# Performance work log

Measured on AMD Instinct MI355X. Metric: run time of the kernel, lower is better.

## Reference

```python
import jax, jax.numpy as jnp
import numpy as np

N_NODES = 50000
N_EDGES = 300000
D = 256
N_RELS = 500


def setup_inputs() -> dict:
    key = jax.random.key(0)
    ks = jax.random.split(key, 12)
    s = 1.0 / np.sqrt(D)  # keep activations O(1) through the dense transforms
    return {
        "h": jax.random.normal(ks[0], (N_NODES, D), dtype=jnp.float32),
        "prev_h": jax.random.normal(ks[1], (N_NODES, D), dtype=jnp.float32),
        "emb_rel": jax.random.normal(ks[2], (N_RELS, D), dtype=jnp.float32),
        "norm": jax.random.uniform(ks[3], (N_NODES, 1), dtype=jnp.float32),
        "weight_neighbor": jax.random.normal(ks[4], (D, D), dtype=jnp.float32) * s,
        "loop_weight": jax.random.normal(ks[5], (D, D), dtype=jnp.float32) * s,
        "evolve_loop_weight": jax.random.normal(ks[6], (D, D), dtype=jnp.float32) * s,
        "skip_connect_weight": jax.random.normal(ks[7], (D, D), dtype=jnp.float32) * s,
        "skip_connect_bias": jnp.zeros((D,), dtype=jnp.float32),
        "src": jax.random.randint(ks[8], (N_EDGES,), 0, N_NODES),
        "dst": jax.random.randint(ks[9], (N_EDGES,), 0, N_NODES),
        "etype": jax.random.randint(ks[10], (N_EDGES,), 0, N_RELS),
    }


def reference(h, prev_h, emb_rel, norm, weight_neighbor, loop_weight,
              evolve_loop_weight, skip_connect_weight, skip_connect_bias,
              src, dst, etype):
    n_nodes = h.shape[0]
    # msg_func: per-edge gather of src features + relation embedding, dense transform
    msg = (h[src] + emb_rel[etype]) @ weight_neighbor          # [E, D]
    # fn.sum: segment-sum messages into destination nodes
    agg = jax.ops.segment_sum(msg, dst, num_segments=n_nodes)  # [N, D]
    # apply_func: multiply by per-node norm
    agg = agg * norm
    # self-loop: loop_weight where in_degree > 0, evolve_loop_weight otherwise
    in_deg = jax.ops.segment_sum(jnp.ones_like(dst), dst, num_segments=n_nodes)
    has_in = (in_deg > 0)[:, None]
    loop_message = jnp.where(has_in, h @ loop_weight, h @ evolve_loop_weight)
    # skip connection gate
    skip_weight = jax.nn.sigmoid(prev_h @ skip_connect_weight + skip_connect_bias)
    node_repr = skip_weight * (agg + loop_message) + (1.0 - skip_weight) * prev_h
    return jax.nn.relu(node_repr)
```

## Files before the change

kernel.cpp:

```cpp
#include <hip/hip_runtime.h>
#include <hip/hip_bf16.h>
#include <cstdint>
#include <cstddef>

#define N_NODES 50000
#define N_EDGES 300000
#define DIM     256
#define KTOT    768
#define N_RELS  500

#define SCAN_BLK  256
#define SCAN_NBLK ((N_NODES + SCAN_BLK - 1) / SCAN_BLK)

typedef unsigned short u16;
typedef __attribute__((ext_vector_type(8))) short short8v;
typedef __attribute__((ext_vector_type(4))) float float4v;

static __device__ __forceinline__ u16 f2bf(float f) {
    union { float f; unsigned u; } v; v.f = f;
    unsigned u = v.u;
    unsigned r = u + 0x7FFFu + ((u >> 16) & 1u);
    return (u16)(r >> 16);
}
static __device__ __forceinline__ float bf2f(u16 b) {
    union { unsigned u; float f; } v; v.u = ((unsigned)b) << 16; return v.f;
}

__global__ void conv_kernel(const float* __restrict__ h, const float* __restrict__ emb,
                            u16* __restrict__ Xh, u16* __restrict__ embb) {
    int i = blockIdx.x * blockDim.x + threadIdx.x;
    int e0 = i * 8;
    if (e0 >= (N_NODES + N_RELS) * DIM) return;
    const float* src; u16* dst; int off;
    if (e0 < N_NODES * DIM) { src = h;   dst = Xh;   off = e0; }
    else                    { src = emb; dst = embb; off = e0 - N_NODES * DIM; }
    float4 a = *(const float4*)(src + off);
    float4 b = *(const float4*)(src + off + 4);
    u16 o[8] = { f2bf(a.x), f2bf(a.y), f2bf(a.z), f2bf(a.w),
                 f2bf(b.x), f2bf(b.y), f2bf(b.z), f2bf(b.w) };
    *(uint4*)(dst + off) = *(const uint4*)o;
}

__global__ void wt_kernel(const float* __restrict__ Wn, const float* __restrict__ Wl,
                          const float* __restrict__ Wsc, u16* __restrict__ Wt) {
    int k = blockIdx.x;
    int d = threadIdx.x;
    const float* W = (k < 256) ? Wn : ((k < 512) ? Wl : Wsc);
    int kk = k & 255;
    Wt[(size_t)d * KTOT + k] = f2bf(W[kk * DIM + d]);
}

__global__ void hist_kernel(const int* __restrict__ dstv, int* __restrict__ deg) {
    int e = blockIdx.x * 256 + threadIdx.x;
    if (e < N_EDGES) atomicAdd(&deg[dstv[e]], 1);
}

__global__ void scanA_kernel(const int* __restrict__ deg, int* __restrict__ excl_local,
                             int* __restrict__ block_sum) {
    __shared__ int sdata[SCAN_BLK];
    int t = threadIdx.x, i = blockIdx.x * SCAN_BLK + t;
    int v = (i < N_NODES) ? deg[i] : 0;
    sdata[t] = v;
    __syncthreads();
    for (int off = 1; off < SCAN_BLK; off <<= 1) {
        int u = (t >= off) ? sdata[t - off] : 0;
        __syncthreads();
        sdata[t] += u;
        __syncthreads();
    }
    if (i < N_NODES) excl_local[i] = sdata[t] - v;
    if (t == SCAN_BLK - 1) block_sum[blockIdx.x] = sdata[t];
}

__global__ void scanB_kernel(const int* __restrict__ block_sum, int* __restrict__ block_base,
                             int* __restrict__ offsets) {
    __shared__ int sdata[SCAN_NBLK];
    int t = threadIdx.x;
    int v = (t < SCAN_NBLK) ? block_sum[t] : 0;
    if (t < SCAN_NBLK) sdata[t] = v;
    __syncthreads();
    for (int off = 1; off < SCAN_NBLK; off <<= 1) {
        int u = (t >= off && t < SCAN_NBLK) ? sdata[t - off] : 0;
        __syncthreads();
        if (t < SCAN_NBLK) sdata[t] += u;
        __syncthreads();
    }
    if (t < SCAN_NBLK) block_base[t] = sdata[t] - v;
    if (t == SCAN_NBLK - 1) offsets[N_NODES] = sdata[t];
}

__global__ void scanC_kernel(const int* __restrict__ excl_local, const int* __restrict__ block_base,
                             int* __restrict__ offsets, int* __restrict__ cursor) {
    int i = blockIdx.x * SCAN_BLK + threadIdx.x;
    if (i < N_NODES) {
        int e = block_base[blockIdx.x] + excl_local[i];
        offsets[i] = e; cursor[i] = e;
    }
}

__global__ void scatter_kernel(const int* __restrict__ src, const int* __restrict__ dstv,
                               const int* __restrict__ et, int* __restrict__ cursor,
                               unsigned* __restrict__ esee) {
    int e = blockIdx.x * 256 + threadIdx.x;
    if (e >= N_EDGES) return;
    int d = dstv[e];
    int pos = atomicAdd(&cursor[d], 1);
    esee[pos] = (unsigned)src[e] * N_RELS + (unsigned)et[e];
}

__global__ void agg_kernel(const u16* __restrict__ Xh, const u16* __restrict__ embb,
                           const float* __restrict__ norm, const int* __restrict__ offsets,
                           const unsigned* __restrict__ esee,
                           u16* __restrict__ Xa, int* __restrict__ wl_count, int* __restrict__ wl) {
    int wave = (blockIdx.x * 256 + threadIdx.x) >> 6;
    int lane = threadIdx.x & 63;
    if (wave >= N_NODES) return;
    int n = wave;
    int s0 = offsets[n], s1 = offsets[n + 1];
    int c4 = lane * 4;
    float4 acc = make_float4(0.f, 0.f, 0.f, 0.f);
    for (int e = s0; e < s1; e++) {
        unsigned v = esee[e];
        unsigned s = v / N_RELS;
        unsigned t = v - s * N_RELS;
        ushort4 hv = *(const ushort4*)(Xh   + (size_t)s * DIM + c4);
        ushort4 ev = *(const ushort4*)(embb + (size_t)t * DIM + c4);
        acc.x += bf2f(hv.x) + bf2f(ev.x);
        acc.y += bf2f(hv.y) + bf2f(ev.y);
        acc.z += bf2f(hv.z) + bf2f(ev.z);
        acc.w += bf2f(hv.w) + bf2f(ev.w);
    }
    float nr = norm[n];
    u16 o[4] = { f2bf(acc.x * nr), f2bf(acc.y * nr), f2bf(acc.z * nr), f2bf(acc.w * nr) };
    *(ushort4*)(Xa + (size_t)n * DIM + c4) = *(const ushort4*)o;
    if (lane == 0 && s1 == s0) { int idx = atomicAdd(wl_count, 1); wl[idx] = n; }
}

#define LDSP 72
__launch_bounds__(256, 2)
__global__ void gemm_kernel(const u16* __restrict__ Xa, const u16* __restrict__ Xh,
                            const u16* __restrict__ Wt, const float* __restrict__ prev_h,
                            const float* __restrict__ bias, float* __restrict__ out) {
    __shared__ u16 Xs[64 * LDSP];
    __shared__ u16 Ws[256 * LDSP];
    int tid = threadIdx.x;
    int wave = tid >> 6, lane = tid & 63, q = lane >> 4, m16 = lane & 15;
    int wn = wave * 64;
    int m0 = blockIdx.x * 64;

    float4v acc1[4][4], acc2[4][4];
#pragma unroll
    for (int i = 0; i < 4; i++)
#pragma unroll
        for (int j = 0; j < 4; j++) { acc1[i][j] = (float4v)0.f; acc2[i][j] = (float4v)0.f; }

    int xr = tid >> 3, xc = (tid & 7) * 8;
    int wp = tid & 7,  wd = tid >> 3;
    int xrow0 = min(m0 + xr, N_NODES - 1);
    int xrow1 = min(m0 + xr + 32, N_NODES - 1);

    for (int kt = 0; kt < 12; kt++) {
        int koff = (kt & 3) * 64;
        if (kt < 8) {
            const u16* Xsrc = (kt < 4) ? Xa : Xh;
            *(uint4*)(&Xs[xr * LDSP + xc]) =
                *(const uint4*)(Xsrc + (size_t)xrow0 * DIM + koff + xc);
            *(uint4*)(&Xs[(xr + 32) * LDSP + xc]) =
                *(const uint4*)(Xsrc + (size_t)xrow1 * DIM + koff + xc);
        } else {
            const float* p0 = prev_h + (size_t)xrow0 * DIM + koff + xc;
            const float* p1 = prev_h + (size_t)xrow1 * DIM + koff + xc;
            float4 a0 = *(const float4*)p0, b0 = *(const float4*)(p0 + 4);
            float4 a1 = *(const float4*)p1, b1 = *(const float4*)(p1 + 4);
            u16 o0[8] = { f2bf(a0.x), f2bf(a0.y), f2bf(a0.z), f2bf(a0.w),
                          f2bf(b0.x), f2bf(b0.y), f2bf(b0.z), f2bf(b0.w) };
            u16 o1[8] = { f2bf(a1.x), f2bf(a1.y), f2bf(a1.z), f2bf(a1.w),
                          f2bf(b1.x), f2bf(b1.y), f2bf(b1.z), f2bf(b1.w) };
            *(uint4*)(&Xs[xr * LDSP + xc])        = *(const uint4*)o0;
            *(uint4*)(&Xs[(xr + 32) * LDSP + xc]) = *(const uint4*)o1;
        }
#pragma unroll
        for (int it = 0; it < 8; it++) {
            int d = wd + it * 32;
            *(uint4*)(&Ws[d * LDSP + wp * 8]) =
                *(const uint4*)(Wt + (size_t)d * KTOT + kt * 64 + wp * 8);
        }
        __syncthreads();
#pragma unroll
        for (int kk = 0; kk < 2; kk++) {
            short8v af[4], bfr[4];
#pragma unroll
            for (int mi = 0; mi < 4; mi++)
                af[mi] = *(const short8v*)(&Xs[(mi * 16 + m16) * LDSP + kk * 32 + q * 8]);
#pragma unroll
            for (int ni = 0; ni < 4; ni++)
                bfr[ni] = *(const short8v*)(&Ws[(wn + ni * 16 + m16) * LDSP + kk * 32 + q * 8]);
            if (kt < 8) {
#pragma unroll
                for (int mi = 0; mi < 4; mi++)
#pragma unroll
                    for (int ni = 0; ni < 4; ni++)
                        acc1[mi][ni] = __builtin_amdgcn_mfma_f32_16x16x32_bf16(
                            af[mi], bfr[ni], acc1[mi][ni], 0, 0, 0);
            } else {
#pragma unroll
                for (int mi = 0; mi < 4; mi++)
#pragma unroll
                    for (int ni = 0; ni < 4; ni++)
                        acc2[mi][ni] = __builtin_amdgcn_mfma_f32_16x16x32_bf16(
                            af[mi], bfr[ni], acc2[mi][ni], 0, 0, 0);
            }
        }
        __syncthreads();
    }

#pragma unroll
    for (int mi = 0; mi < 4; mi++) {
#pragma unroll
        for (int ni = 0; ni < 4; ni++) {
            int d = wn + ni * 16 + m16;
            float b = bias[d];
#pragma unroll
            for (int r = 0; r < 4; r++) {
                int node = m0 + mi * 16 + q * 4 + r;
                if (node < N_NODES) {
                    float S  = acc2[mi][ni][r] + b;
                    float sw = 1.f / (1.f + __expf(-S));
                    float ph = prev_h[(size_t)node * DIM + d];
                    float v  = sw * acc1[mi][ni][r] + (1.f - sw) * ph;
                    out[(size_t)node * DIM + d] = fmaxf(v, 0.f);
                }
            }
        }
    }
}

__global__ void fixup_kernel(const float* __restrict__ h, const float* __restrict__ prev_h,
                             const float* __restrict__ We, const float* __restrict__ Wsc,
                             const float* __restrict__ bias, const int* __restrict__ wl_count,
                             const int* __restrict__ wl, float* __restrict__ out) {
    __shared__ float ph[DIM], hh[DIM];
    int d = threadIdx.x;
    int cnt = *wl_count;
    for (int i = blockIdx.x; i < cnt; i += gridDim.x) {
        int n = wl[i];
        ph[d] = prev_h[(size_t)n * DIM + d];
        hh[d] = h[(size_t)n * DIM + d];
        __syncthreads();
        float s = 0.f, l = 0.f;
        for (int k = 0; k < DIM; k++) {
            s += ph[k] * Wsc[k * DIM + d];
            l += hh[k] * We[k * DIM + d];
        }
        float sw = 1.f / (1.f + __expf(-(s + bias[d])));
        float v = sw * l + (1.f - sw) * ph[d];
        out[(size_t)n * DIM + d] = fmaxf(v, 0.f);
        __syncthreads();
    }
}

extern "C" void kernel_launch(void* const* d_in, const int* in_sizes, int n_in,
                              void* d_out, int out_size, void* d_ws, size_t ws_size,
                              hipStream_t stream) {
    const float* h      = (const float*)d_in[0];
    const float* prev_h = (const float*)d_in[1];
    const float* emb    = (const float*)d_in[2];
    const float* norm   = (const float*)d_in[3];
    const float* Wn     = (const float*)d_in[4];
    const float* Wl     = (const float*)d_in[5];
    const float* We     = (const float*)d_in[6];
    const float* Wsc    = (const float*)d_in[7];
    const float* bias   = (const float*)d_in[8];
    const int*   src    = (const int*)d_in[9];
    const int*   dstv   = (const int*)d_in[10];
    const int*   et     = (const int*)d_in[11];
    float* out = (float*)d_out;

    char* ws = (char*)d_ws;
    size_t off = 0;
    auto alloc = [&](size_t bytes) -> char* {
        char* p = ws + off; off += (bytes + 255) & ~(size_t)255; return p;
    };
    u16* Xa      = (u16*)alloc((size_t)N_NODES * DIM * 2);
    u16* Xh      = (u16*)alloc((size_t)N_NODES * DIM * 2);
    u16* embb    = (u16*)alloc((size_t)N_RELS * DIM * 2);
    u16* Wt      = (u16*)alloc((size_t)DIM * KTOT * 2);
    int* deg     = (int*)alloc((size_t)N_NODES * 4);
    int* wlcnt   = (int*)alloc(16);
    int* wl      = (int*)alloc((size_t)N_NODES * 4);
    int* offsets = (int*)alloc((size_t)(N_NODES + 1) * 4);
    int* cursor  = (int*)alloc((size_t)N_NODES * 4);
    unsigned* esee = (unsigned*)alloc((size_t)N_EDGES * 4);
    int* excl    = (int*)alloc((size_t)N_NODES * 4);
    int* bsum    = (int*)alloc((size_t)SCAN_NBLK * 4);
    int* bbase   = (int*)alloc((size_t)SCAN_NBLK * 4);

    hipMemsetAsync(deg, 0, (size_t)N_NODES * 4, stream);
    hipMemsetAsync(wlcnt, 0, 4, stream);

    conv_kernel<<<((N_NODES + N_RELS) * DIM / 8 + 255) / 256, 256, 0, stream>>>(h, emb, Xh, embb);
    wt_kernel<<<KTOT, 256, 0, stream>>>(Wn, Wl, Wsc, Wt);
    hist_kernel<<<(N_EDGES + 255) / 256, 256, 0, stream>>>(dstv, deg);
    scanA_kernel<<<SCAN_NBLK, SCAN_BLK, 0, stream>>>(deg, excl, bsum);
    scanB_kernel<<<1, SCAN_BLK, 0, stream>>>(bsum, bbase, offsets);
    scanC_kernel<<<SCAN_NBLK, SCAN_BLK, 0, stream>>>(excl, bbase, offsets, cursor);
    scatter_kernel<<<(N_EDGES + 255) / 256, 256, 0, stream>>>(src, dstv, et, cursor, esee);
    agg_kernel<<<(N_NODES + 3) / 4, 256, 0, stream>>>(Xh, embb, norm, offsets, esee, Xa, wlcnt, wl);
    gemm_kernel<<<(N_NODES + 63) / 64, 256, 0, stream>>>(Xa, Xh, Wt, prev_h, bias, out);
    fixup_kernel<<<256, 256, 0, stream>>>(h, prev_h, We, Wsc, bias, wlcnt, wl, out);
}
```

Measured before the change: 348.5 us.

## Double-buffer GEMM via direct global-to-LDS loads with swizzled layout and concatenated X

Rewrites the fused GEMM main loop to double-buffer LDS tiles, filling them with global_load_lds (direct global-to-LDS copies) and an XOR-swizzled layout in place of padded rows, so the next K-tile loads while MFMAs run on the current one. The prev_h tiles are prefetched into registers and converted after compute. The aggregated and raw node features are stored interleaved in one 512-wide buffer so the A operand comes from a single source. The aggregation loop is also unrolled by two edges to raise memory-level parallelism. LDS use grows because of double buffering, which may limit occupancy, and the swizzle/async-load indexing adds correctness risk.

```diff
diff --git a/kernel.cpp b/kernel.cpp
--- a/kernel.cpp
+++ b/kernel.cpp
@@ -1,5 +1,4 @@
 #include <hip/hip_runtime.h>
-#include <hip/hip_bf16.h>
 #include <cstdint>
 #include <cstddef>
 
@@ -26,19 +25,32 @@
     union { unsigned u; float f; } v; v.u = ((unsigned)b) << 16; return v.f;
 }
 
+static __device__ __forceinline__ void gld16(const void* g, u16* l) {
+    __builtin_amdgcn_global_load_lds(
+        (const __attribute__((address_space(1))) unsigned int*)g,
+        (__attribute__((address_space(3))) unsigned int*)l,
+        16, 0, 0);
+}
+
 __global__ void conv_kernel(const float* __restrict__ h, const float* __restrict__ emb,
-                            u16* __restrict__ Xh, u16* __restrict__ embb) {
+                            u16* __restrict__ Xcat, u16* __restrict__ embb) {
     int i = blockIdx.x * blockDim.x + threadIdx.x;
     int e0 = i * 8;
     if (e0 >= (N_NODES + N_RELS) * DIM) return;
-    const float* src; u16* dst; int off;
-    if (e0 < N_NODES * DIM) { src = h;   dst = Xh;   off = e0; }
-    else                    { src = emb; dst = embb; off = e0 - N_NODES * DIM; }
-    float4 a = *(const float4*)(src + off);
-    float4 b = *(const float4*)(src + off + 4);
+    const float* src; u16* dst;
+    if (e0 < N_NODES * DIM) {
+        int n = e0 >> 8, c = e0 & 255;
+        src = h + e0;
+        dst = Xcat + (size_t)n * 512 + 256 + c;
+    } else {
+        int off = e0 - N_NODES * DIM;
+        src = emb + off; dst = embb + off;
+    }
+    float4 a = *(const float4*)(src);
+    float4 b = *(const float4*)(src + 4);
     u16 o[8] = { f2bf(a.x), f2bf(a.y), f2bf(a.z), f2bf(a.w),
                  f2bf(b.x), f2bf(b.y), f2bf(b.z), f2bf(b.w) };
-    *(uint4*)(dst + off) = *(const uint4*)o;
+    *(uint4*)dst = *(const uint4*)o;
 }
 
 __global__ void wt_kernel(const float* __restrict__ Wn, const float* __restrict__ Wl,
@@ -108,10 +120,10 @@
     esee[pos] = (unsigned)src[e] * N_RELS + (unsigned)et[e];
 }
 
-__global__ void agg_kernel(const u16* __restrict__ Xh, const u16* __restrict__ embb,
+__global__ void agg_kernel(u16* __restrict__ Xcat, const u16* __restrict__ embb,
                            const float* __restrict__ norm, const int* __restrict__ offsets,
                            const unsigned* __restrict__ esee,
-                           u16* __restrict__ Xa, int* __restrict__ wl_count, int* __restrict__ wl) {
+                           int* __restrict__ wl_count, int* __restrict__ wl) {
     int wave = (blockIdx.x * 256 + threadIdx.x) >> 6;
     int lane = threadIdx.x & 63;
     if (wave >= N_NODES) return;
@@ -119,11 +131,25 @@
     int s0 = offsets[n], s1 = offsets[n + 1];
     int c4 = lane * 4;
     float4 acc = make_float4(0.f, 0.f, 0.f, 0.f);
-    for (int e = s0; e < s1; e++) {
+    int e = s0;
+    for (; e + 1 < s1; e += 2) {
+        unsigned v0 = esee[e], v1 = esee[e + 1];
+        unsigned sa = v0 / N_RELS, ta = v0 - sa * N_RELS;
+        unsigned sb = v1 / N_RELS, tb = v1 - sb * N_RELS;
+        ushort4 ha = *(const ushort4*)(Xcat + (size_t)sa * 512 + 256 + c4);
+        ushort4 ea = *(const ushort4*)(embb + (size_t)ta * DIM + c4);
+        ushort4 hb = *(const ushort4*)(Xcat + (size_t)sb * 512 + 256 + c4);
+        ushort4 eb = *(const ushort4*)(embb + (size_t)tb * DIM + c4);
+        acc.x += bf2f(ha.x) + bf2f(ea.x) + bf2f(hb.x) + bf2f(eb.x);
+        acc.y += bf2f(ha.y) + bf2f(ea.y) + bf2f(hb.y) + bf2f(eb.y);
+        acc.z += bf2f(ha.z) + bf2f(ea.z) + bf2f(hb.z) + bf2f(eb.z);
+        acc.w += bf2f(ha.w) + bf2f(ea.w) + bf2f(hb.w) + bf2f(eb.w);
+    }
+    if (e < s1) {
         unsigned v = esee[e];
         unsigned s = v / N_RELS;
         unsigned t = v - s * N_RELS;
-        ushort4 hv = *(const ushort4*)(Xh   + (size_t)s * DIM + c4);
+        ushort4 hv = *(const ushort4*)(Xcat + (size_t)s * 512 + 256 + c4);
         ushort4 ev = *(const ushort4*)(embb + (size_t)t * DIM + c4);
         acc.x += bf2f(hv.x) + bf2f(ev.x);
         acc.y += bf2f(hv.y) + bf2f(ev.y);
@@ -132,21 +158,32 @@
     }
     float nr = norm[n];
     u16 o[4] = { f2bf(acc.x * nr), f2bf(acc.y * nr), f2bf(acc.z * nr), f2bf(acc.w * nr) };
-    *(ushort4*)(Xa + (size_t)n * DIM + c4) = *(const ushort4*)o;
+    *(ushort4*)(Xcat + (size_t)n * 512 + c4) = *(const ushort4*)o;
     if (lane == 0 && s1 == s0) { int idx = atomicAdd(wl_count, 1); wl[idx] = n; }
 }
 
-#define LDSP 72
 __launch_bounds__(256, 2)
-__global__ void gemm_kernel(const u16* __restrict__ Xa, const u16* __restrict__ Xh,
-                            const u16* __restrict__ Wt, const float* __restrict__ prev_h,
-                            const float* __restrict__ bias, float* __restrict__ out) {
-    __shared__ u16 Xs[64 * LDSP];
-    __shared__ u16 Ws[256 * LDSP];
-    int tid = threadIdx.x;
+__global__ void gemm_kernel(const u16* __restrict__ Xcat, const u16* __restrict__ Wt,
+                            const float* __restrict__ prev_h, const float* __restrict__ bias,
+                            float* __restrict__ out) {
+    __shared__ __align__(16) u16 lds[40960];
+    int tid  = threadIdx.x;
     int wave = tid >> 6, lane = tid & 63, q = lane >> 4, m16 = lane & 15;
     int wn = wave * 64;
     int m0 = blockIdx.x * 64;
+    int lr = lane >> 3, lc8 = lane & 7;
+    int scol = (lc8 ^ lr) << 3;
+
+    int ar0 = wave * 16 + lr, ar1 = ar0 + 8;
+    int ga0 = (m0 + ar0 < N_NODES) ? (m0 + ar0) : (N_NODES - 1);
+    int ga1 = (m0 + ar1 < N_NODES) ? (m0 + ar1) : (N_NODES - 1);
+    const u16*   sA0 = Xcat   + (size_t)ga0 * 512 + scol;
+    const u16*   sA1 = Xcat   + (size_t)ga1 * 512 + scol;
+    const float* pP0 = prev_h + (size_t)ga0 * 256 + scol;
+    const float* pP1 = prev_h + (size_t)ga1 * 256 + scol;
+    const u16*   sB  = Wt + (size_t)(wave * 64 + lr) * KTOT + scol;
+    int ldsA_w = wave * 16 * 64;
+    int ldsB_w = 8192 + wave * 64 * 64;
 
     float4v acc1[4][4], acc2[4][4];
 #pragma unroll
@@ -154,47 +191,49 @@
 #pragma unroll
         for (int j = 0; j < 4; j++) { acc1[i][j] = (float4v)0.f; acc2[i][j] = (float4v)0.f; }
 
-    int xr = tid >> 3, xc = (tid & 7) * 8;
-    int wp = tid & 7,  wd = tid >> 3;
-    int xrow0 = min(m0 + xr, N_NODES - 1);
-    int xrow1 = min(m0 + xr + 32, N_NODES - 1);
-
+#pragma unroll
+    for (int j = 0; j < 8; j++)
+        gld16(sB + (size_t)j * 8 * KTOT, &lds[ldsB_w + j * 512]);
+    gld16(sA0, &lds[ldsA_w]);
+    gld16(sA1, &lds[ldsA_w + 512]);
+    __syncthreads();
+
+    int sw = (m16 & 7) << 3;
+
+#pragma unroll
     for (int kt = 0; kt < 12; kt++) {
-        int koff = (kt & 3) * 64;
-        if (kt < 8) {
-            const u16* Xsrc = (kt < 4) ? Xa : Xh;
-            *(uint4*)(&Xs[xr * LDSP + xc]) =
-                *(const uint4*)(Xsrc + (size_t)xrow0 * DIM + koff + xc);
-            *(uint4*)(&Xs[(xr + 32) * LDSP + xc]) =
-                *(const uint4*)(Xsrc + (size_t)xrow1 * DIM + koff + xc);
-        } else {
-            const float* p0 = prev_h + (size_t)xrow0 * DIM + koff + xc;
-            const float* p1 = prev_h + (size_t)xrow1 * DIM + koff + xc;
-            float4 a0 = *(const float4*)p0, b0 = *(const float4*)(p0 + 4);
-            float4 a1 = *(const float4*)p1, b1 = *(const float4*)(p1 + 4);
-            u16 o0[8] = { f2bf(a0.x), f2bf(a0.y), f2bf(a0.z), f2bf(a0.w),
-                          f2bf(b0.x), f2bf(b0.y), f2bf(b0.z), f2bf(b0.w) };
-            u16 o1[8] = { f2bf(a1.x), f2bf(a1.y), f2bf(a1.z), f2bf(a1.w),
-                          f2bf(b1.x), f2bf(b1.y), f2bf(b1.z), f2bf(b1.w) };
-            *(uint4*)(&Xs[xr * LDSP + xc])        = *(const uint4*)o0;
-            *(uint4*)(&Xs[(xr + 32) * LDSP + xc]) = *(const uint4*)o1;
-        }
-#pragma unroll
-        for (int it = 0; it < 8; it++) {
-            int d = wd + it * 32;
-            *(uint4*)(&Ws[d * LDSP + wp * 8]) =
-                *(const uint4*)(Wt + (size_t)d * KTOT + kt * 64 + wp * 8);
-        }
-        __syncthreads();
+        int buf = kt & 1, nbuf = buf ^ 1;
+        float pf0[8], pf1[8];
+        if (kt < 11) {
+            int kn = kt + 1;
+#pragma unroll
+            for (int j = 0; j < 8; j++)
+                gld16(sB + (size_t)j * 8 * KTOT + kn * 64,
+                      &lds[ldsB_w + nbuf * 16384 + j * 512]);
+            if (kn < 8) {
+                gld16(sA0 + kn * 64, &lds[ldsA_w + nbuf * 4096]);
+                gld16(sA1 + kn * 64, &lds[ldsA_w + nbuf * 4096 + 512]);
+            } else {
+                const float* p0 = pP0 + (kn - 8) * 64;
+                const float* p1 = pP1 + (kn - 8) * 64;
+                float4 x0 = *(const float4*)p0, y0 = *(const float4*)(p0 + 4);
+                float4 x1 = *(const float4*)p1, y1 = *(const float4*)(p1 + 4);
+                pf0[0] = x0.x; pf0[1] = x0.y; pf0[2] = x0.z; pf0[3] = x0.w;
+                pf0[4] = y0.x; pf0[5] = y0.y; pf0[6] = y0.z; pf0[7] = y0.w;
+                pf1[0] = x1.x; pf1[1] = x1.y; pf1[2] = x1.z; pf1[3] = x1.w;
+                pf1[4] = y1.x; pf1[5] = y1.y; pf1[6] = y1.z; pf1[7] = y1.w;
+            }
+        }
 #pragma unroll
         for (int kk = 0; kk < 2; kk++) {
+            int ck = (kk * 32 + q * 8) ^ sw;
             short8v af[4], bfr[4];
 #pragma unroll
             for (int mi = 0; mi < 4; mi++)
-                af[mi] = *(const short8v*)(&Xs[(mi * 16 + m16) * LDSP + kk * 32 + q * 8]);
+                af[mi] = *(const short8v*)(&lds[buf * 4096 + (mi * 16 + m16) * 64 + ck]);
 #pragma unroll
             for (int ni = 0; ni < 4; ni++)
-                bfr[ni] = *(const short8v*)(&Ws[(wn + ni * 16 + m16) * LDSP + kk * 32 + q * 8]);
+                bfr[ni] = *(const short8v*)(&lds[8192 + buf * 16384 + (wn + ni * 16 + m16) * 64 + ck]);
             if (kt < 8) {
 #pragma unroll
                 for (int mi = 0; mi < 4; mi++)
@@ -211,6 +250,14 @@
                             af[mi], bfr[ni], acc2[mi][ni], 0, 0, 0);
             }
         }
+        if (kt < 11 && kt + 1 >= 8) {
+            u16 o0[8] = { f2bf(pf0[0]), f2bf(pf0[1]), f2bf(pf0[2]), f2bf(pf0[3]),
+                          f2bf(pf0[4]), f2bf(pf0[5]), f2bf(pf0[6]), f2bf(pf0[7]) };
+            u16 o1[8] = { f2bf(pf1[0]), f2bf(pf1[1]), f2bf(pf1[2]), f2bf(pf1[3]),
+                          f2bf(pf1[4]), f2bf(pf1[5]), f2bf(pf1[6]), f2bf(pf1[7]) };
+            *(uint4*)(&lds[nbuf * 4096 + ar0 * 64 + lc8 * 8]) = *(const uint4*)o0;
+            *(uint4*)(&lds[nbuf * 4096 + ar1 * 64 + lc8 * 8]) = *(const uint4*)o1;
+        }
         __syncthreads();
     }
 
@@ -225,9 +272,9 @@
                 int node = m0 + mi * 16 + q * 4 + r;
                 if (node < N_NODES) {
                     float S  = acc2[mi][ni][r] + b;
-                    float sw = 1.f / (1.f + __expf(-S));
+                    float sg = 1.f / (1.f + __expf(-S));
                     float ph = prev_h[(size_t)node * DIM + d];
-                    float v  = sw * acc1[mi][ni][r] + (1.f - sw) * ph;
+                    float v  = sg * acc1[mi][ni][r] + (1.f - sg) * ph;
                     out[(size_t)node * DIM + d] = fmaxf(v, 0.f);
                 }
             }
@@ -252,8 +299,8 @@
             s += ph[k] * Wsc[k * DIM + d];
             l += hh[k] * We[k * DIM + d];
         }
-        float sw = 1.f / (1.f + __expf(-(s + bias[d])));
-        float v = sw * l + (1.f - sw) * ph[d];
+        float sg = 1.f / (1.f + __expf(-(s + bias[d])));
+        float v = sg * l + (1.f - sg) * ph[d];
         out[(size_t)n * DIM + d] = fmaxf(v, 0.f);
         __syncthreads();
     }
@@ -281,8 +328,7 @@
     auto alloc = [&](size_t bytes) -> char* {
         char* p = ws + off; off += (bytes + 255) & ~(size_t)255; return p;
     };
-    u16* Xa      = (u16*)alloc((size_t)N_NODES * DIM * 2);
-    u16* Xh      = (u16*)alloc((size_t)N_NODES * DIM * 2);
+    u16* Xcat    = (u16*)alloc((size_t)N_NODES * 512 * 2);
     u16* embb    = (u16*)alloc((size_t)N_RELS * DIM * 2);
     u16* Wt      = (u16*)alloc((size_t)DIM * KTOT * 2);
     int* deg     = (int*)alloc((size_t)N_NODES * 4);
@@ -298,14 +344,14 @@
     hipMemsetAsync(deg, 0, (size_t)N_NODES * 4, stream);
     hipMemsetAsync(wlcnt, 0, 4, stream);
 
-    conv_kernel<<<((N_NODES + N_RELS) * DIM / 8 + 255) / 256, 256, 0, stream>>>(h, emb, Xh, embb);
+    conv_kernel<<<((N_NODES + N_RELS) * DIM / 8 + 255) / 256, 256, 0, stream>>>(h, emb, Xcat, embb);
     wt_kernel<<<KTOT, 256, 0, stream>>>(Wn, Wl, Wsc, Wt);
     hist_kernel<<<(N_EDGES + 255) / 256, 256, 0, stream>>>(dstv, deg);
     scanA_kernel<<<SCAN_NBLK, SCAN_BLK, 0, stream>>>(deg, excl, bsum);
     scanB_kernel<<<1, SCAN_BLK, 0, stream>>>(bsum, bbase, offsets);
     scanC_kernel<<<SCAN_NBLK, SCAN_BLK, 0, stream>>>(excl, bbase, offsets, cursor);
     scatter_kernel<<<(N_EDGES + 255) / 256, 256, 0, stream>>>(src, dstv, et, cursor, esee);
-    agg_kernel<<<(N_NODES + 3) / 4, 256, 0, stream>>>(Xh, embb, norm, offsets, esee, Xa, wlcnt, wl);
-    gemm_kernel<<<(N_NODES + 63) / 64, 256, 0, stream>>>(Xa, Xh, Wt, prev_h, bias, out);
+    agg_kernel<<<(N_NODES + 3) / 4, 256, 0, stream>>>(Xcat, embb, norm, offsets, esee, wlcnt, wl);
+    gemm_kernel<<<(N_NODES + 63) / 64, 256, 0, stream>>>(Xcat, Wt, prev_h, bias, out);
     fixup_kernel<<<256, 256, 0, stream>>>(h, prev_h, We, Wsc, bias, wlcnt, wl, out);
 }
```

New measurement: 317.7 us. 1.1x faster.
